# Performance work log

Measured on AMD Instinct MI355X. Metric: run time of the kernel, lower is better.

The kernel has to match this reference:

```python
import jax, jax.numpy as jnp
import numpy as np

N_NODES = 4194304  # 2**22
LEVELS = 10
COARSE = 8192
RANK = 2
NNZ = 8388608


def _interp_linear(u, N):
    """torch F.interpolate(mode='linear', align_corners=False) along axis 1. u: (B,M,R) -> (B,N,R)."""
    M = u.shape[1]
    pos = (jnp.arange(N, dtype=jnp.float32) + 0.5) * (M / N) - 0.5
    pos = jnp.clip(pos, 0.0, M - 1)
    i0 = jnp.floor(pos).astype(jnp.int32)
    i1 = jnp.minimum(i0 + 1, M - 1)
    w = (pos - i0.astype(jnp.float32))[None, :, None]
    return u[:, i0] * (1.0 - w) + u[:, i1] * w


def _apply_hodlr(diag, u_factors, v_factors, x):
    B, N, _ = x.shape
    y = diag * x
    L = u_factors.shape[0]
    for lvl in range(L):
        num_splits = 2 ** (lvl + 1)
        bs = N // num_splits
        if bs == 0:
            continue
        uc, vc = u_factors[lvl], v_factors[lvl]
        u_full = _interp_linear(uc, N) if uc.shape[1] != N else uc
        v_full = _interp_linear(vc, N) if vc.shape[1] != N else vc
        P = num_splits // 2
        valid = P * 2 * bs
        xv = x[:, :valid].reshape(B, P, 2, bs, 1)
        uv = u_full[:, :valid].reshape(B, P, 2, bs, -1)
        vv = v_full[:, :valid].reshape(B, P, 2, bs, -1)
        xL, xR = xv[:, :, 0], xv[:, :, 1]
        uL, uR = uv[:, :, 0], uv[:, :, 1]
        vL, vR = vv[:, :, 0], vv[:, :, 1]
        xRp = jnp.einsum('bpkr,bpko->bpro', vR, xR)  # (B,P,R,1)
        xLp = jnp.einsum('bpkr,bpko->bpro', vL, xL)
        yL = jnp.einsum('bpkr,bpro->bpko', uL, xRp)  # (B,P,bs,1)
        yR = jnp.einsum('bpkr,bpro->bpko', uR, xLp)
        upd = jnp.stack([yL, yR], axis=2).reshape(B, valid, 1)
        if valid < N:
            upd = jnp.pad(upd, ((0, 0), (0, N - valid), (0, 0)))
        y = y + upd
    return y


def setup_inputs() -> dict:
    key = jax.random.key(0)
    ks = jax.random.split(key, 6)
    diag = jax.random.uniform(ks[0], (1, N_NODES, 1), dtype=jnp.float32)
    u_factors = jax.random.normal(ks[1], (LEVELS, 1, COARSE, RANK), dtype=jnp.float32)
    v_factors = jax.random.normal(ks[2], (LEVELS, 1, COARSE, RANK), dtype=jnp.float32)
    A_values = jax.random.normal(ks[3], (NNZ,), dtype=jnp.float32)
    z = jax.random.normal(ks[4], (1, N_NODES, 1), dtype=jnp.float32)
    A_indices = jax.random.randint(ks[5], (2, NNZ), 0, N_NODES, dtype=jnp.int64) if jax.config.jax_enable_x64 else jax.random.randint(ks[5], (2, NNZ), 0, N_NODES, dtype=jnp.int32)
    return {"diag": diag, "u_factors": u_factors, "v_factors": v_factors,
            "A_values": A_values, "z": z, "A_indices": A_indices, "num_nodes": N_NODES}


def reference(diag, u_factors, v_factors, A_values, z, A_indices, num_nodes):
    N = num_nodes
    w = _apply_hodlr(diag, u_factors, v_factors, z)          # (1,N,1)
    w_flat = w.reshape(N)
    rows, cols = A_indices[0], A_indices[1]
    y_flat = jax.ops.segment_sum(A_values * w_flat[cols], rows, num_segments=N)
    y = y_flat.reshape(1, N, 1)
    loss = jnp.mean((y - z) ** 2)
    return loss
```

## Files before the change

### kernel.cpp

```cpp
#include <hip/hip_runtime.h>

#define N_NODES 4194304
#define LEVELS  10
#define COARSE  8192
#define NNZ_E   8388608
#define NSEG    512
#define RB_SZ   8192
#define EPB     8192
#define CAP_SEG 18432u

typedef int          v4i __attribute__((ext_vector_type(4)));
typedef float        v4f __attribute__((ext_vector_type(4)));
typedef unsigned int v4u __attribute__((ext_vector_type(4)));

static __device__ __forceinline__ unsigned short f2bf(float x) {
    unsigned u = __float_as_uint(x);
    return (unsigned short)((u + 0x7FFFu + ((u >> 16) & 1u)) >> 16);
}
static __device__ __forceinline__ float bf2f(unsigned short h) {
    return __uint_as_float((unsigned)h << 16);
}

__global__ __launch_bounds__(512) void k1(const float* __restrict__ z,
                                          float2* __restrict__ M,
                                          float* __restrict__ S,
                                          float* __restrict__ out,
                                          unsigned* __restrict__ segCtr) {
    int b = blockIdx.x, t = threadIdx.x;
    if (b == 0) {
        for (int i = t; i < 2046 * 2; i += 512) S[i] = 0.f;
        if (t == 0) out[0] = 0.f;
        segCtr[t] = 0u;
    }
    int lane = t & 63, wave = t >> 6;
    int chunk = b * 8 + wave;
    int base = chunk * 256 + lane * 4;
    float4 zv = *(const float4*)(z + base);
    float a0 = 0.f, a1 = 0.f;
    const float* zp = (const float*)&zv;
#pragma unroll
    for (int j = 0; j < 4; ++j) {
        float p = ((float)(base + j) + 0.5f) * (1.0f / 512.0f) - 0.5f;
        p = fminf(fmaxf(p, 0.0f), (float)(COARSE - 1));
        float f = p - floorf(p);
        a0 += zp[j] * (1.0f - f);
        a1 += zp[j] * f;
    }
#pragma unroll
    for (int off = 32; off >= 1; off >>= 1) {
        a0 += __shfl_xor(a0, off, 64);
        a1 += __shfl_xor(a1, off, 64);
    }
    if (lane == 0) M[chunk] = make_float2(a0, a1);
}

__global__ __launch_bounds__(256) void kB(const float2* __restrict__ M,
                                          const float* __restrict__ V,
                                          float* __restrict__ S) {
    int b = blockIdx.x, t = threadIdx.x;
    int lvl = b >> 3, slice = b & 7;
    const float2* Vl = (const float2*)(V + lvl * COARSE * 2);
    float s0 = 0.f, s1 = 0.f;
    int c0 = slice * 2048 + t * 8;
#pragma unroll
    for (int cc = 0; cc < 8; ++cc) {
        int c = c0 + cc;
        float2 m = M[c];
        int k = (c > 0) ? ((c - 1) >> 1) : 0;
        int kp = min(k + 1, COARSE - 1);
        float2 vk = Vl[k], vkp = Vl[kp];
        s0 += vk.x * m.x + vkp.x * m.y;
        s1 += vk.y * m.x + vkp.y * m.y;
    }
    int gw = min(1 << (10 - lvl), 64);
    for (int sh = gw >> 1; sh >= 1; sh >>= 1) {
        s0 += __shfl_xor(s0, sh, 64);
        s1 += __shfl_xor(s1, sh, 64);
    }
    if ((t & (gw - 1)) == 0) {
        int bb = c0 >> (13 - lvl);
        int soff = (2 << lvl) - 2;
        unsafeAtomicAdd(&S[(soff + bb) * 2 + 0], s0);
        unsafeAtomicAdd(&S[(soff + bb) * 2 + 1], s1);
    }
}

__global__ __launch_bounds__(512) void kCw(const float* __restrict__ diag,
                                           const float* __restrict__ z,
                                           const float* __restrict__ S,
                                           const float* __restrict__ U,
                                           unsigned short* __restrict__ wb) {
    int b = blockIdx.x, t = threadIdx.x;
    int tid = b * 512 + t;
    int base = tid * 4;
    int c = base >> 8;
    int k = (c > 0) ? ((c - 1) >> 1) : 0;
    int kp = min(k + 1, COARSE - 1);
    float g0 = 0.f, g1 = 0.f;
#pragma unroll
    for (int lvl = 0; lvl < LEVELS; ++lvl) {
        int sib = (c >> (13 - lvl)) ^ 1;
        int soff = (2 << lvl) - 2;
        float2 s2 = ((const float2*)S)[soff + sib];
        const float2* Ul = (const float2*)(U + lvl * COARSE * 2);
        float2 uk = Ul[k], ukp = Ul[kp];
        g0 += uk.x * s2.x + uk.y * s2.y;
        g1 += ukp.x * s2.x + ukp.y * s2.y;
    }
    float4 d4 = *(const float4*)(diag + base);
    float4 z4 = *(const float4*)(z + base);
    const float* dp = (const float*)&d4;
    const float* zp = (const float*)&z4;
    ushort4 h4;
    unsigned short* hp = (unsigned short*)&h4;
#pragma unroll
    for (int j = 0; j < 4; ++j) {
        float p = ((float)(base + j) + 0.5f) * (1.0f / 512.0f) - 0.5f;
        p = fminf(fmaxf(p, 0.0f), (float)(COARSE - 1));
        float f = p - floorf(p);
        hp[j] = f2bf(dp[j] * zp[j] + (g0 + f * (g1 - g0)));
    }
    *(ushort4*)(wb + base) = h4;
}

__global__ __launch_bounds__(512) void kG(const int* __restrict__ cols,
                                          const float* __restrict__ vals,
                                          const unsigned short* __restrict__ wb,
                                          float* __restrict__ wp) {
    int b = blockIdx.x, t = threadIdx.x;
    int base = b * 4096;
    v4i c[2];
    v4f v[2];
#pragma unroll
    for (int j = 0; j < 2; ++j) {
        int e = base + j * 2048 + t * 4;
        c[j] = __builtin_nontemporal_load((const v4i*)(cols + e));
        v[j] = __builtin_nontemporal_load((const v4f*)(vals + e));
    }
    float wf[8];
#pragma unroll 1
    for (int p = 0; p < 4; ++p) {
#pragma unroll
        for (int j = 0; j < 2; ++j) {
            const int* cp = (const int*)&c[j];
#pragma unroll
            for (int kk = 0; kk < 4; ++kk) {
                unsigned cc = (unsigned)cp[kk];
                if ((cc >> 20) == (unsigned)p)
                    wf[j * 4 + kk] = bf2f(wb[cc]);
            }
        }
        __syncthreads();
    }
#pragma unroll
    for (int j = 0; j < 2; ++j) {
        const float* vp = (const float*)&v[j];
        v4f o;
        float* op = (float*)&o;
#pragma unroll
        for (int kk = 0; kk < 4; ++kk) op[kk] = wf[j * 4 + kk] * vp[kk];
        int e = base + j * 2048 + t * 4;
        __builtin_nontemporal_store(o, (v4f*)(wp + e));
    }
}

__global__ __launch_bounds__(1024) void k2s(const int* __restrict__ rows,
                                            const float* __restrict__ wp,
                                            unsigned* __restrict__ segCtr,
                                            unsigned* __restrict__ binned) {
    __shared__ unsigned sortedP[EPB];
    __shared__ unsigned short sortedB[EPB];
    __shared__ unsigned cur[NSEG], gb[NSEG];
    __shared__ unsigned wsum[16], wbase[16];
    int blk = blockIdx.x, t = threadIdx.x;
    int base = blk * EPB;
    v4i r[2];
    v4f p4[2];
#pragma unroll
    for (int j = 0; j < 2; ++j) {
        int e = base + j * 4096 + t * 4;
        r[j] = __builtin_nontemporal_load((const v4i*)(rows + e));
        p4[j] = __builtin_nontemporal_load((const v4f*)(wp + e));
    }
    if (t < NSEG) cur[t] = 0u;
    __syncthreads();
#pragma unroll
    for (int j = 0; j < 2; ++j) {
        const int* rp = (const int*)&r[j];
#pragma unroll
        for (int kk = 0; kk < 4; ++kk)
            atomicAdd(&cur[(unsigned)rp[kk] >> 13], 1u);
    }
    __syncthreads();
    unsigned lv = 0, lincl = 0;
    if (t < NSEG) {
        lv = cur[t];
        lincl = lv;
#pragma unroll
        for (int off = 1; off < 64; off <<= 1) {
            unsigned n = __shfl_up(lincl, off, 64);
            if ((t & 63) >= off) lincl += n;
        }
        if ((t & 63) == 63) wsum[t >> 6] = lincl;
    }
    __syncthreads();
    if (t == 0) {
        unsigned a = 0;
        for (int i = 0; i < 8; ++i) { wbase[i] = a; a += wsum[i]; }
    }
    __syncthreads();
    if (t < NSEG) {
        unsigned lexcl = wbase[t >> 6] + lincl - lv;
        gb[t] = (unsigned)t * CAP_SEG + atomicAdd(&segCtr[t], lv) - lexcl;
        cur[t] = lexcl;
    }
    __syncthreads();
#pragma unroll
    for (int j = 0; j < 2; ++j) {
        const int* rp = (const int*)&r[j];
        const float* pp = (const float*)&p4[j];
#pragma unroll
        for (int kk = 0; kk < 4; ++kk) {
            unsigned row = (unsigned)rp[kk];
            unsigned seg = row >> 13;
            unsigned rl = row & 8191u;
            unsigned pe = ((__float_as_uint(pp[kk]) + 0x1000u) >> 13) & 0x7FFFFu;
            unsigned i = atomicAdd(&cur[seg], 1u);
            sortedP[i] = (rl << 19) | pe;
            sortedB[i] = (unsigned short)seg;
        }
    }
    __syncthreads();
#pragma unroll
    for (int k = 0; k < 8; ++k) {
        int i = k * 1024 + t;
        unsigned s = sortedB[i];
        __builtin_nontemporal_store(sortedP[i], binned + gb[s] + i);
    }
}

__global__ __launch_bounds__(1024) void kE(const unsigned* __restrict__ binned,
                                           const unsigned* __restrict__ segCtr,
                                           const float* __restrict__ z,
                                           float* __restrict__ out) {
    __shared__ float acc[RB_SZ];
    __shared__ float red[16];
    int b = blockIdx.x, t = threadIdx.x;

    for (int i = t; i < RB_SZ / 4; i += 1024) ((float4*)acc)[i] = make_float4(0.f, 0.f, 0.f, 0.f);
    __syncthreads();

    unsigned n = segCtr[b];
    const unsigned* seg = binned + (size_t)b * CAP_SEG;
    unsigned i = t;
    for (; i + 7u * 1024u < n; i += 8u * 1024u) {
        unsigned ev[8];
#pragma unroll
        for (int k = 0; k < 8; ++k)
            ev[k] = __builtin_nontemporal_load(seg + i + (unsigned)k * 1024u);
#pragma unroll
        for (int k = 0; k < 8; ++k)
            atomicAdd(&acc[ev[k] >> 19], __uint_as_float((ev[k] & 0x7FFFFu) << 13));
    }
    for (; i < n; i += 1024u) {
        unsigned e = __builtin_nontemporal_load(seg + i);
        atomicAdd(&acc[e >> 19], __uint_as_float((e & 0x7FFFFu) << 13));
    }
    __syncthreads();

    float part = 0.f;
    int gbase = b * RB_SZ;
    for (int k = t; k < RB_SZ; k += 1024) {
        float d = acc[k] - z[gbase + k];
        part += d * d;
    }
#pragma unroll
    for (int off = 32; off >= 1; off >>= 1) part += __shfl_xor(part, off, 64);
    if ((t & 63) == 0) red[t >> 6] = part;
    __syncthreads();
    if (t == 0) {
        float s = 0.f;
        for (int k = 0; k < 16; ++k) s += red[k];
        unsafeAtomicAdd(out, s * (1.0f / (float)N_NODES));
    }
}

extern "C" void kernel_launch(void* const* d_in, const int* in_sizes, int n_in,
                              void* d_out, int out_size, void* d_ws, size_t ws_size,
                              hipStream_t stream) {
    const float* diag  = (const float*)d_in[0];
    const float* U     = (const float*)d_in[1];
    const float* V     = (const float*)d_in[2];
    const float* Avals = (const float*)d_in[3];
    const float* z     = (const float*)d_in[4];
    const int*   Aidx  = (const int*)d_in[5];
    const int* rows = Aidx;
    const int* cols = Aidx + NNZ_E;

    char* ws = (char*)d_ws;
    size_t off = 0;
    unsigned short* wb  = (unsigned short*)(ws + off); off += (size_t)N_NODES * 2;
    unsigned* binned    = (unsigned*)(ws + off);       off += (size_t)NSEG * CAP_SEG * 4;
    float* wp           = (float*)(ws + off);          off += (size_t)NNZ_E * 4;
    unsigned* segCtr    = (unsigned*)(ws + off);       off += NSEG * 4;
    float2* M           = (float2*)(ws + off);         off += (size_t)(N_NODES / 256) * 8;
    float* S            = (float*)(ws + off);          off += 16384;

    k1<<<2048, 512, 0, stream>>>(z, M, S, (float*)d_out, segCtr);
    kB<<<80, 256, 0, stream>>>(M, V, S);
    kCw<<<2048, 512, 0, stream>>>(diag, z, S, U, wb);
    kG<<<2048, 512, 0, stream>>>(cols, Avals, wb, wp);
    k2s<<<1024, 1024, 0, stream>>>(rows, wp, segCtr, binned);
    kE<<<NSEG, 1024, 0, stream>>>(binned, segCtr, z, (float*)d_out);
}
```

Measured before the change: 304.2 us.

## Scatter binned entries directly to global and double per-block work in gather

The binning kernel no longer stages a locally sorted copy in shared memory with a prefix scan. Each thread now takes its global slot with an atomic on a shared per-segment cursor that is seeded from the global segment counter, and writes the packed entry straight to the binned buffer. Both the gather and binning kernels now process 8192 edges per 512-thread block. This removes the shared sort, the scan and several barriers, but turns the output into scattered, uncoalesced global stores and raises per-thread register use.

```diff
diff --git a/kernel.cpp b/kernel.cpp
--- a/kernel.cpp
+++ b/kernel.cpp
@@ -128,20 +128,20 @@
                                           const unsigned short* __restrict__ wb,
                                           float* __restrict__ wp) {
     int b = blockIdx.x, t = threadIdx.x;
-    int base = b * 4096;
-    v4i c[2];
-    v4f v[2];
-#pragma unroll
-    for (int j = 0; j < 2; ++j) {
+    int base = b * EPB;
+    v4i c[4];
+    v4f v[4];
+#pragma unroll
+    for (int j = 0; j < 4; ++j) {
         int e = base + j * 2048 + t * 4;
         c[j] = __builtin_nontemporal_load((const v4i*)(cols + e));
         v[j] = __builtin_nontemporal_load((const v4f*)(vals + e));
     }
-    float wf[8];
+    float wf[16];
 #pragma unroll 1
     for (int p = 0; p < 4; ++p) {
 #pragma unroll
-        for (int j = 0; j < 2; ++j) {
+        for (int j = 0; j < 4; ++j) {
             const int* cp = (const int*)&c[j];
 #pragma unroll
             for (int kk = 0; kk < 4; ++kk) {
@@ -153,7 +153,7 @@
         __syncthreads();
     }
 #pragma unroll
-    for (int j = 0; j < 2; ++j) {
+    for (int j = 0; j < 4; ++j) {
         const float* vp = (const float*)&v[j];
         v4f o;
         float* op = (float*)&o;
@@ -164,59 +164,38 @@
     }
 }
 
-__global__ __launch_bounds__(1024) void k2s(const int* __restrict__ rows,
-                                            const float* __restrict__ wp,
-                                            unsigned* __restrict__ segCtr,
-                                            unsigned* __restrict__ binned) {
-    __shared__ unsigned sortedP[EPB];
-    __shared__ unsigned short sortedB[EPB];
-    __shared__ unsigned cur[NSEG], gb[NSEG];
-    __shared__ unsigned wsum[16], wbase[16];
+__global__ __launch_bounds__(512) void kS(const int* __restrict__ rows,
+                                          const float* __restrict__ wp,
+                                          unsigned* __restrict__ segCtr,
+                                          unsigned* __restrict__ binned) {
+    __shared__ unsigned cur[NSEG];
     int blk = blockIdx.x, t = threadIdx.x;
     int base = blk * EPB;
-    v4i r[2];
-    v4f p4[2];
-#pragma unroll
-    for (int j = 0; j < 2; ++j) {
-        int e = base + j * 4096 + t * 4;
+    v4i r[4];
+    v4f p4[4];
+#pragma unroll
+    for (int j = 0; j < 4; ++j) {
+        int e = base + j * 2048 + t * 4;
         r[j] = __builtin_nontemporal_load((const v4i*)(rows + e));
         p4[j] = __builtin_nontemporal_load((const v4f*)(wp + e));
     }
-    if (t < NSEG) cur[t] = 0u;
-    __syncthreads();
-#pragma unroll
-    for (int j = 0; j < 2; ++j) {
+    cur[t] = 0u;
+    __syncthreads();
+#pragma unroll
+    for (int j = 0; j < 4; ++j) {
         const int* rp = (const int*)&r[j];
 #pragma unroll
         for (int kk = 0; kk < 4; ++kk)
             atomicAdd(&cur[(unsigned)rp[kk] >> 13], 1u);
     }
     __syncthreads();
-    unsigned lv = 0, lincl = 0;
-    if (t < NSEG) {
-        lv = cur[t];
-        lincl = lv;
-#pragma unroll
-        for (int off = 1; off < 64; off <<= 1) {
-            unsigned n = __shfl_up(lincl, off, 64);
-            if ((t & 63) >= off) lincl += n;
-        }
-        if ((t & 63) == 63) wsum[t >> 6] = lincl;
-    }
-    __syncthreads();
-    if (t == 0) {
-        unsigned a = 0;
-        for (int i = 0; i < 8; ++i) { wbase[i] = a; a += wsum[i]; }
-    }
-    __syncthreads();
-    if (t < NSEG) {
-        unsigned lexcl = wbase[t >> 6] + lincl - lv;
-        gb[t] = (unsigned)t * CAP_SEG + atomicAdd(&segCtr[t], lv) - lexcl;
-        cur[t] = lexcl;
-    }
-    __syncthreads();
-#pragma unroll
-    for (int j = 0; j < 2; ++j) {
+    {
+        unsigned lv = cur[t];
+        cur[t] = (unsigned)t * CAP_SEG + atomicAdd(&segCtr[t], lv);
+    }
+    __syncthreads();
+#pragma unroll
+    for (int j = 0; j < 4; ++j) {
         const int* rp = (const int*)&r[j];
         const float* pp = (const float*)&p4[j];
 #pragma unroll
@@ -225,17 +204,9 @@
             unsigned seg = row >> 13;
             unsigned rl = row & 8191u;
             unsigned pe = ((__float_as_uint(pp[kk]) + 0x1000u) >> 13) & 0x7FFFFu;
-            unsigned i = atomicAdd(&cur[seg], 1u);
-            sortedP[i] = (rl << 19) | pe;
-            sortedB[i] = (unsigned short)seg;
+            unsigned pos = atomicAdd(&cur[seg], 1u);
+            binned[pos] = (rl << 19) | pe;
         }
-    }
-    __syncthreads();
-#pragma unroll
-    for (int k = 0; k < 8; ++k) {
-        int i = k * 1024 + t;
-        unsigned s = sortedB[i];
-        __builtin_nontemporal_store(sortedP[i], binned + gb[s] + i);
     }
 }
 
@@ -309,7 +280,7 @@
     k1<<<2048, 512, 0, stream>>>(z, M, S, (float*)d_out, segCtr);
     kB<<<80, 256, 0, stream>>>(M, V, S);
     kCw<<<2048, 512, 0, stream>>>(diag, z, S, U, wb);
-    kG<<<2048, 512, 0, stream>>>(cols, Avals, wb, wp);
-    k2s<<<1024, 1024, 0, stream>>>(rows, wp, segCtr, binned);
+    kG<<<1024, 512, 0, stream>>>(cols, Avals, wb, wp);
+    kS<<<1024, 512, 0, stream>>>(rows, wp, segCtr, binned);
     kE<<<NSEG, 1024, 0, stream>>>(binned, segCtr, z, (float*)d_out);
 }
```

New measurement: 308.4 us. No clear change (+1.4%).
